# Optimization experiments

Hardware: AMD Instinct MI355X
Metric: run time of the kernel (lower is better)

Reference implementation:

```python
import jax, jax.numpy as jnp
import numpy as np

B, T, V, D = 4, 2048, 2048, 512

def setup_inputs() -> dict:
    key = jax.random.key(0)
    ks = jax.random.split(key, 8)
    x = jax.random.normal(ks[0], (B, T, V), dtype=jnp.float32)
    Wq = 0.02 * jax.random.normal(ks[1], (V, D), dtype=jnp.float32)
    Wk = 0.02 * jax.random.normal(ks[2], (3, V, D), dtype=jnp.float32)
    Wv = 0.02 * jax.random.normal(ks[3], (3, V, D), dtype=jnp.float32)
    Wo = 0.02 * jax.random.normal(ks[4], (D, V), dtype=jnp.float32)
    Wg = 0.02 * jax.random.normal(ks[5], (V, 3), dtype=jnp.float32)
    decay_logits = jnp.array([0.0, 3.0, 5.0], dtype=jnp.float32)
    out_scale = jnp.float32(0.1)
    return {"x": x, "Wq": Wq, "Wk": Wk, "Wv": Wv, "Wo": Wo, "Wg": Wg,
            "decay_logits": decay_logits, "out_scale": out_scale}

def reference(x, Wq, Wk, Wv, Wo, Wg, decay_logits, out_scale):
    # x: [B, T, V]
    Tn = x.shape[1]
    q = x @ Wq                                   # [B, T, D]
    gate = jax.nn.softmax(x @ Wg, axis=-1)       # [B, T, 3]
    pos = jnp.arange(Tn)
    diff = pos[None, :] - pos[:, None]           # diff[i, j] = j - i (as in torch code)
    causal = (diff > 0).astype(x.dtype)          # nonzero when j > i (faithful to source)
    expn = jnp.maximum(diff - 1, 0).astype(x.dtype)  # [T, T]
    blended = jnp.zeros(q.shape, dtype=x.dtype)
    for i in range(3):  # small fixed loop over 3 scales
        k = x @ Wk[i]                            # [B, T, D]
        v = x @ Wv[i]                            # [B, T, D]
        decay = jax.nn.sigmoid(decay_logits[i])
        w = (decay ** expn) * causal             # [T, T] decay mask
        scores = jnp.einsum('btd,bsd->bts', q, k) * w[None]  # [B, T, T]
        retrieved = jnp.einsum('bts,bsd->btd', scores, v)     # [B, T, D]
        blended = blended + gate[..., i:i + 1] * retrieved
    return (blended @ Wo) * out_scale            # [B, T, V]
```

## Files before the change

### kernel.cpp

```cpp
#include <hip/hip_runtime.h>
#include <hip/hip_bf16.h>
#include <cstdint>

typedef __attribute__((ext_vector_type(8))) short short8;
typedef __attribute__((ext_vector_type(4))) float f32x4;

#define DEV static __device__ __forceinline__

DEV unsigned short f2bf(float f) {
  uint32_t u = __float_as_uint(f);
  uint32_t r = (u + 0x7FFFu + ((u >> 16) & 1u)) >> 16;
  return (unsigned short)r;
}
DEV float bf2f(unsigned short v) { return __uint_as_float((uint32_t)v << 16); }

DEV unsigned short to_bf(float v) { return f2bf(v); }
DEV unsigned short to_bf(unsigned short v) { return v; }

DEV void async_copy16(const unsigned short* g, unsigned short* l) {
  __builtin_amdgcn_global_load_lds(
      (const __attribute__((address_space(1))) void*)g,
      (__attribute__((address_space(3))) void*)l, 16, 0, 0);
}

DEV int xcd_swizzle(int orig, int nwg) {
  int q = nwg >> 3, r = nwg & 7;
  int xcd = orig & 7, idx = orig >> 3;
  return (xcd < r ? xcd * (q + 1) : r * (q + 1) + (xcd - r) * q) + idx;
}

DEV void band_info(const float* __restrict__ dl, int T, int scale_idx, int zb, int ZB,
                   long& off, int& W, float& l2d) {
  off = 0; W = 0; l2d = 0.f;
  #pragma unroll
  for (int i = 0; i < 3; ++i) {
    float dlv = dl[i];
    float dc = 1.f / (1.f + expf(-dlv));
    float l2 = log2f(dc);
    float bf_ = 16.f / fmaxf(-l2, 1e-9f) + 129.f;
    int bt = (bf_ >= (float)T) ? T : ((int)ceilf(bf_ / 128.f)) * 128;
    if (bt > T) bt = T;
    int Wi = min(bt + 128, T);
    if (i < scale_idx) off += (long)ZB * T * Wi;
    if (i == scale_idx) { W = Wi; l2d = l2; }
  }
  off += (long)zb * (long)T * W;
}

__global__ __launch_bounds__(256) void convert_gate(
    const float* __restrict__ x, const float* __restrict__ Wg,
    unsigned short* __restrict__ xb, float* __restrict__ gate) {
  const int row = blockIdx.x;
  const float* xr = x + (long)row * 2048;
  unsigned short* xo = xb + (long)row * 2048;
  const int tid = threadIdx.x;
  float a0 = 0.f, a1 = 0.f, a2 = 0.f;
  #pragma unroll
  for (int u = 0; u < 2; ++u) {
    int c = u * 1024 + tid * 4;
    float4 v = *(const float4*)&xr[c];
    ushort4 o;
    o.x = f2bf(v.x); o.y = f2bf(v.y); o.z = f2bf(v.z); o.w = f2bf(v.w);
    *(ushort4*)&xo[c] = o;
    float vv[4] = {v.x, v.y, v.z, v.w};
    #pragma unroll
    for (int e = 0; e < 4; ++e) {
      a0 += vv[e] * Wg[(c + e) * 3 + 0];
      a1 += vv[e] * Wg[(c + e) * 3 + 1];
      a2 += vv[e] * Wg[(c + e) * 3 + 2];
    }
  }
  #pragma unroll
  for (int off = 32; off; off >>= 1) {
    a0 += __shfl_xor(a0, off);
    a1 += __shfl_xor(a1, off);
    a2 += __shfl_xor(a2, off);
  }
  __shared__ float red[3][4];
  const int w = tid >> 6, lane = tid & 63;
  if (lane == 0) { red[0][w] = a0; red[1][w] = a1; red[2][w] = a2; }
  __syncthreads();
  if (tid == 0) {
    float s0 = red[0][0] + red[0][1] + red[0][2] + red[0][3];
    float s1 = red[1][0] + red[1][1] + red[1][2] + red[1][3];
    float s2 = red[2][0] + red[2][1] + red[2][2] + red[2][3];
    float m = fmaxf(s0, fmaxf(s1, s2));
    float e0 = expf(s0 - m), e1 = expf(s1 - m), e2 = expf(s2 - m);
    float s = 1.f / (e0 + e1 + e2);
    gate[row * 3 + 0] = e0 * s;
    gate[row * 3 + 1] = e1 * s;
    gate[row * 3 + 2] = e2 * s;
  }
}

__global__ __launch_bounds__(256) void transpose_qkv_weights(
    const float* __restrict__ Wq, const float* __restrict__ Wk,
    const float* __restrict__ Wv, unsigned short* __restrict__ wall,
    int V, int D) {
  __shared__ unsigned short tile[32][33];
  const int z = blockIdx.z;
  const float* src = (z == 0) ? Wq
                   : (z < 4) ? Wk + (long)(z - 1) * V * D
                             : Wv + (long)(z - 4) * V * D;
  unsigned short* dst = wall + (long)z * D * V;
  int c0 = blockIdx.x * 32, r0 = blockIdx.y * 32;
  int tx = threadIdx.x & 31, ty = threadIdx.x >> 5;
  #pragma unroll
  for (int k = 0; k < 4; k++) {
    int rr = ty + k * 8;
    tile[rr][tx] = f2bf(src[(long)(r0 + rr) * D + c0 + tx]);
  }
  __syncthreads();
  #pragma unroll
  for (int k = 0; k < 4; k++) {
    int cc = ty + k * 8;
    dst[(long)(c0 + cc) * V + r0 + tx] = tile[tx][cc];
  }
}

template<typename TIN>
__global__ __launch_bounds__(256) void transpose_to_bf16(const TIN* __restrict__ src,
                                                         unsigned short* __restrict__ dst,
                                                         int R, int C, int ldS,
                                                         long sS_lo, long sS_hi, int ZB,
                                                         long sD) {
  __shared__ unsigned short tile[32][33];
  int z = blockIdx.z;
  src += (long)(z % ZB) * sS_lo + (long)(z / ZB) * sS_hi;
  dst += (long)z * sD;
  int c0 = blockIdx.x * 32, r0 = blockIdx.y * 32;
  int tx = threadIdx.x & 31, ty = threadIdx.x >> 5;
  #pragma unroll
  for (int k = 0; k < 4; k++) {
    int rr = ty + k * 8;
    tile[rr][tx] = to_bf(src[(long)(r0 + rr) * ldS + c0 + tx]);
  }
  __syncthreads();
  #pragma unroll
  for (int k = 0; k < 4; k++) {
    int cc = ty + k * 8;
    dst[(long)(c0 + cc) * R + r0 + tx] = tile[tx][cc];
  }
}

__global__ __launch_bounds__(256) void sum3_bf16(const unsigned short* __restrict__ r,
                                                 long n, long stride,
                                                 unsigned short* __restrict__ out) {
  long i = ((long)blockIdx.x * 256 + threadIdx.x) * 8;
  if (i >= n) return;
  short8 v0 = *(const short8*)&r[i];
  short8 v1 = *(const short8*)&r[i + stride];
  short8 v2 = *(const short8*)&r[i + 2 * stride];
  short8 o;
  #pragma unroll
  for (int e = 0; e < 8; ++e) {
    float s = bf2f((unsigned short)v0[e]) + bf2f((unsigned short)v1[e]) +
              bf2f((unsigned short)v2[e]);
    o[e] = (short)f2bf(s);
  }
  *(short8*)&out[i] = o;
}

DEV void core128(const unsigned short* A, const unsigned short* Bt,
                 int lda, int ldb, int m0, int n0,
                 int kaoff, int kboff, int kstart, int kend,
                 unsigned short* ldsbuf, int w, int lane,
                 f32x4 (&acc)[4][4]) {
  const int rl = w * 8 + (lane >> 3);
  const int colel = ((lane & 7) ^ (lane >> 3)) << 3;
  const int lr = lane & 15, g = lane >> 4;
  const int wm = w >> 1, wn = w & 1;
  unsigned short* aBuf = ldsbuf;
  unsigned short* bBuf = ldsbuf + 8192;

  for (int k0 = kstart; k0 < kend; k0 += 64) {
    #pragma unroll
    for (int s = 0; s < 4; ++s)
      async_copy16(A + (long)(m0 + s * 32 + rl) * lda + kaoff + k0 + colel,
                   aBuf + ((s * 4096 + w * 1024) >> 1));
    #pragma unroll
    for (int s = 0; s < 4; ++s)
      async_copy16(Bt + (long)(n0 + s * 32 + rl) * ldb + kboff + k0 + colel,
                   bBuf + ((s * 4096 + w * 1024) >> 1));
    __syncthreads();
    #pragma unroll
    for (int ks = 0; ks < 2; ++ks) {
      const int cb = (ks * 64 + g * 16) ^ ((lr & 7) << 4);
      short8 af[4], bf[4];
      #pragma unroll
      for (int i = 0; i < 4; ++i)
        af[i] = *(const short8*)((const char*)aBuf + (wm * 64 + i * 16 + lr) * 128 + cb);
      #pragma unroll
      for (int j = 0; j < 4; ++j)
        bf[j] = *(const short8*)((const char*)bBuf + (wn * 64 + j * 16 + lr) * 128 + cb);
      #pragma unroll
      for (int i = 0; i < 4; ++i)
        #pragma unroll
        for (int j = 0; j < 4; ++j)
          acc[i][j] = __builtin_amdgcn_mfma_f32_16x16x32_bf16(af[i], bf[j], acc[i][j], 0, 0, 0);
    }
    __syncthreads();
  }
}

__global__ __launch_bounds__(256) void scores_kernel(
    const unsigned short* __restrict__ qkv, unsigned short* __restrict__ sbc,
    int T, int D, int NP, int B, const float* __restrict__ dl) {
  const int z = blockIdx.z;
  const int zb = z % B, scale = z / B;
  const int m0 = blockIdx.y * 128;
  long off; int W; float l2d;
  band_info(dl, T, scale, zb, B, off, W, l2d);
  const int n0_rel = blockIdx.x * 128;
  if (n0_rel >= W) return;
  const int n0 = m0 + n0_rel;
  if (n0 >= T) return;

  const unsigned short* A  = qkv + (long)zb * T * NP;
  const unsigned short* Bt = qkv + (long)zb * T * NP + (1 + scale) * 512;

  __shared__ __align__(16) unsigned short lds[16384];
  const int tid = threadIdx.x;
  const int w = tid >> 6, lane = tid & 63;
  const int lr = lane & 15, g = lane >> 4;
  const int wm = w >> 1, wn = w & 1;

  f32x4 acc[4][4];
  #pragma unroll
  for (int i = 0; i < 4; i++)
    #pragma unroll
    for (int j = 0; j < 4; j++) acc[i][j] = (f32x4){0.f, 0.f, 0.f, 0.f};

  core128(A, Bt, NP, NP, m0, n0, 0, 0, 0, D, lds, w, lane, acc);

  unsigned short* C = sbc + off;
  const int orow = m0 + wm * 64;
  const int ocol_rel = n0_rel + wn * 64;
  #pragma unroll
  for (int i = 0; i < 4; i++)
    #pragma unroll
    for (int j = 0; j < 4; j++)
      #pragma unroll
      for (int e = 0; e < 4; e++) {
        int t = orow + i * 16 + g * 4 + e;
        int s_rel = ocol_rel + j * 16 + lr;
        int s_abs = m0 + s_rel;
        float wgt = (s_abs > t) ? exp2f(l2d * (float)(s_abs - t - 1)) : 0.f;
        C[(long)t * W + s_rel] = f2bf(acc[i][j][e] * wgt);
      }
}

__global__ __launch_bounds__(256) void retr_kernel(
    const unsigned short* __restrict__ sbc, const unsigned short* __restrict__ vT3,
    unsigned short* __restrict__ ret3, const float* __restrict__ gate,
    int T, int D, int B, const float* __restrict__ dl) {
  const int z = blockIdx.z;
  const int zb = z % B, scale = z / B;
  const int m0 = blockIdx.y * 128;
  const int n0 = blockIdx.x * 128;
  long off; int W; float l2d;
  band_info(dl, T, scale, zb, B, off, W, l2d);
  const int kend = min(W, T - m0);

  const unsigned short* A  = sbc + off;
  const unsigned short* Bt = vT3 + (long)z * D * T;

  __shared__ __align__(16) unsigned short lds[16384];
  const int tid = threadIdx.x;
  const int w = tid >> 6, lane = tid & 63;
  const int lr = lane & 15, g = lane >> 4;
  const int wm = w >> 1, wn = w & 1;

  f32x4 acc[4][4];
  #pragma unroll
  for (int i = 0; i < 4; i++)
    #pragma unroll
    for (int j = 0; j < 4; j++) acc[i][j] = (f32x4){0.f, 0.f, 0.f, 0.f};

  core128(A, Bt, W, T, m0, n0, 0, m0, 0, kend, lds, w, lane, acc);

  unsigned short* C2 = ret3 + (long)z * T * D;
  const int orow = m0 + wm * 64;
  const int ocol = n0 + wn * 64;
  #pragma unroll
  for (int i = 0; i < 4; i++) {
    #pragma unroll
    for (int e = 0; e < 4; e++) {
      int t = orow + i * 16 + g * 4 + e;
      float gv = gate[((long)zb * T + t) * 3 + scale];
      #pragma unroll
      for (int j = 0; j < 4; j++) {
        int d = ocol + j * 16 + lr;
        C2[(long)t * D + d] = f2bf(gv * acc[i][j][e]);
      }
    }
  }
}

__global__ __launch_bounds__(256) void gemm128_scale(
    const unsigned short* __restrict__ A, const unsigned short* __restrict__ Bt,
    float* __restrict__ C, int M, int N, int K, int lda, int ldb, int ldc,
    const float* __restrict__ out_scale) {
  int nwg = gridDim.x * gridDim.y;
  int orig = blockIdx.y * gridDim.x + blockIdx.x;
  int wg = xcd_swizzle(orig, nwg);
  const int m0 = (wg / gridDim.x) * 128;
  const int n0 = (wg % gridDim.x) * 128;

  __shared__ __align__(16) unsigned short lds[16384];
  const int tid = threadIdx.x;
  const int w = tid >> 6, lane = tid & 63;
  const int lr = lane & 15, g = lane >> 4;
  const int wm = w >> 1, wn = w & 1;

  f32x4 acc[4][4];
  #pragma unroll
  for (int i = 0; i < 4; i++)
    #pragma unroll
    for (int j = 0; j < 4; j++) acc[i][j] = (f32x4){0.f, 0.f, 0.f, 0.f};

  core128(A, Bt, lda, ldb, m0, n0, 0, 0, 0, K, lds, w, lane, acc);

  const float sc = *out_scale;
  const int orow = m0 + wm * 64;
  const int ocol = n0 + wn * 64;
  #pragma unroll
  for (int i = 0; i < 4; i++)
    #pragma unroll
    for (int j = 0; j < 4; j++)
      #pragma unroll
      for (int e = 0; e < 4; e++) {
        int r = orow + i * 16 + g * 4 + e;
        int c = ocol + j * 16 + lr;
        C[(long)r * ldc + c] = acc[i][j][e] * sc;
      }
}

enum { EPI_BF16 = 0, EPI_SCALE_F32 = 3 };

DEV void stage_pair(const unsigned short* P, int ldp, int base, int k0,
                    int w, int rl, int colel, unsigned short* dst, int s0) {
  async_copy16(P + (long)(base + s0 * 64 + rl) * ldp + k0 + colel,
               dst + ((s0 * 8192 + w * 1024) >> 1));
  async_copy16(P + (long)(base + (s0 + 1) * 64 + rl) * ldp + k0 + colel,
               dst + (((s0 + 1) * 8192 + w * 1024) >> 1));
}

DEV void ds_read_A4(const unsigned short* As, int wm, int lr, int cb, int h,
                    short8 (&af)[4]) {
  #pragma unroll
  for (int ii = 0; ii < 4; ++ii)
    af[ii] = *(const short8*)((const char*)As + (wm * 128 + (h * 4 + ii) * 16 + lr) * 128 + cb);
}

DEV void ds_read_B4(const unsigned short* Bs, int wn, int lr, int cb, short8 (&bf)[4]) {
  #pragma unroll
  for (int jj = 0; jj < 4; ++jj)
    bf[jj] = *(const short8*)((const char*)Bs + (wn * 64 + jj * 16 + lr) * 128 + cb);
}

DEV void mfma16(const short8 (&af)[4], const short8 (&bf)[4], int h, f32x4 (&acc)[8][4]) {
  __builtin_amdgcn_s_setprio(1);
  #pragma unroll
  for (int ii = 0; ii < 4; ++ii)
    #pragma unroll
    for (int jj = 0; jj < 4; ++jj)
      acc[h * 4 + ii][jj] =
          __builtin_amdgcn_mfma_f32_16x16x32_bf16(af[ii], bf[jj], acc[h * 4 + ii][jj], 0, 0, 0);
  __builtin_amdgcn_s_setprio(0);
}

template<bool STAGE>
DEV void tile_phases(const unsigned short* As, const unsigned short* Bs,
                     const unsigned short* A, const unsigned short* Bt,
                     int lda, int ldb, int m0, int n0, int k1,
                     int w, int rl, int colel, unsigned short* bufn,
                     int wm, int wn, int lr, int g, f32x4 (&acc)[8][4]) {
  short8 afA[4], afB[4], bfA[4], bfB[4];
  const int cb0 = (g * 16) ^ ((lr & 7) << 4);
  const int cb1 = (64 + g * 16) ^ ((lr & 7) << 4);

  asm volatile("s_waitcnt vmcnt(0)" ::: "memory");
  __builtin_amdgcn_s_barrier();
  __builtin_amdgcn_sched_barrier(0);

  ds_read_A4(As, wm, lr, cb0, 0, afA);
  ds_read_B4(Bs, wn, lr, cb0, bfA);

  ds_read_A4(As, wm, lr, cb0, 1, afB);
  if (STAGE) {
    stage_pair(A, lda, m0, k1, w, rl, colel, bufn, 0);
    stage_pair(A, lda, m0, k1, w, rl, colel, bufn, 2);
  }
  asm volatile("s_waitcnt lgkmcnt(4)" ::: "memory");
  __builtin_amdgcn_sched_barrier(0);
  mfma16(afA, bfA, 0, acc);
  __builtin_amdgcn_s_barrier();

  ds_read_A4(As, wm, lr, cb1, 0, afA);
  ds_read_B4(Bs, wn, lr, cb1, bfB);
  if (STAGE) {
    stage_pair(Bt, ldb, n0, k1, w, rl, colel, bufn + 16384, 0);
    stage_pair(Bt, ldb, n0, k1, w, rl, colel, bufn + 16384, 2);
  }
  asm volatile("s_waitcnt lgkmcnt(8)" ::: "memory");
  __builtin_amdgcn_sched_barrier(0);
  mfma16(afB, bfA, 1, acc);
  __builtin_amdgcn_s_barrier();

  ds_read_A4(As, wm, lr, cb1, 1, afB);
  asm volatile("s_waitcnt lgkmcnt(4)" ::: "memory");
  __builtin_amdgcn_sched_barrier(0);
  mfma16(afA, bfB, 0, acc);
  __builtin_amdgcn_s_barrier();

  asm volatile("s_waitcnt lgkmcnt(0)" ::: "memory");
  __builtin_amdgcn_sched_barrier(0);
  mfma16(afB, bfB, 1, acc);
  __builtin_amdgcn_s_barrier();
}

DEV void stage_tile256(const unsigned short* A, const unsigned short* Bt,
                       int lda, int ldb, int m0, int n0, int k0,
                       int w, int rl, int colel, unsigned short* buf) {
  #pragma unroll
  for (int s = 0; s < 4; ++s)
    async_copy16(A + (long)(m0 + s * 64 + rl) * lda + k0 + colel,
                 buf + ((s * 8192 + w * 1024) >> 1));
  #pragma unroll
  for (int s = 0; s < 4; ++s)
    async_copy16(Bt + (long)(n0 + s * 64 + rl) * ldb + k0 + colel,
                 buf + 16384 + ((s * 8192 + w * 1024) >> 1));
}

template<int EPI, int SWZ>
__global__ __launch_bounds__(512) void gemm256(
    const unsigned short* __restrict__ A, const unsigned short* __restrict__ Bt,
    void* __restrict__ Cv, int M, int N, int K, int lda, int ldb, int ldc,
    const float* __restrict__ out_scale) {
  __shared__ __align__(16) unsigned short lds[65536];
  int m0, n0;
  {
    int gx = gridDim.x;
    int orig = blockIdx.y * gx + blockIdx.x;
    int wg = SWZ ? xcd_swizzle(orig, gx * gridDim.y) : orig;
    m0 = (wg / gx) * 256;
    n0 = (wg % gx) * 256;
  }
  const int tid = threadIdx.x;
  const int w = tid >> 6, lane = tid & 63;
  const int wm = w >> 2, wn = w & 3;
  const int lr = lane & 15, g = lane >> 4;
  const int rl = w * 8 + (lane >> 3);
  const int colel = ((lane & 7) ^ (lane >> 3)) << 3;

  f32x4 acc[8][4];
  #pragma unroll
  for (int i = 0; i < 8; ++i)
    #pragma unroll
    for (int j = 0; j < 4; ++j) acc[i][j] = (f32x4){0.f, 0.f, 0.f, 0.f};

  const int nkt = K >> 6;
  stage_tile256(A, Bt, lda, ldb, m0, n0, 0, w, rl, colel, lds);
  int cur = 0;
  for (int t = 0; t < nkt - 1; ++t) {
    const unsigned short* As = lds + (cur << 15);
    unsigned short* bufn = lds + ((cur ^ 1) << 15);
    tile_phases<true>(As, As + 16384, A, Bt, lda, ldb, m0, n0, (t + 1) << 6,
                      w, rl, colel, bufn, wm, wn, lr, g, acc);
    cur ^= 1;
  }
  {
    const unsigned short* As = lds + (cur << 15);
    tile_phases<false>(As, As + 16384, A, Bt, lda, ldb, m0, n0, 0,
                       w, rl, colel, nullptr, wm, wn, lr, g, acc);
  }

  const int orow = m0 + wm * 128;
  const int ocol = n0 + wn * 64;
  if (EPI == EPI_BF16) {
    unsigned short* C = (unsigned short*)Cv;
    #pragma unroll
    for (int i = 0; i < 8; ++i)
      #pragma unroll
      for (int j = 0; j < 4; ++j)
        #pragma unroll
        for (int e = 0; e < 4; ++e)
          C[(long)(orow + i * 16 + g * 4 + e) * ldc + ocol + j * 16 + lr] = f2bf(acc[i][j][e]);
  } else {
    float sc = *out_scale;
    float* C = (float*)Cv;
    #pragma unroll
    for (int i = 0; i < 8; ++i)
      #pragma unroll
      for (int j = 0; j < 4; ++j)
        #pragma unroll
        for (int e = 0; e < 4; ++e)
          C[(long)(orow + i * 16 + g * 4 + e) * ldc + ocol + j * 16 + lr] = acc[i][j][e] * sc;
  }
}

extern "C" void kernel_launch(void* const* d_in, const int* in_sizes, int n_in,
                              void* d_out, int out_size, void* d_ws, size_t ws_size,
                              hipStream_t stream) {
  const int B = 4, T = 2048, V = 2048, D = 512;
  const int M = B * T;
  const int NP = 7 * D;

  const float* x   = (const float*)d_in[0];
  const float* Wq  = (const float*)d_in[1];
  const float* Wk  = (const float*)d_in[2];
  const float* Wv  = (const float*)d_in[3];
  const float* Wo  = (const float*)d_in[4];
  const float* Wg  = (const float*)d_in[5];
  const float* dl  = (const float*)d_in[6];
  const float* osc = (const float*)d_in[7];

  char* p = (char*)d_ws;
  auto carve = [&](size_t bytes) -> void* {
    void* r = (void*)p;
    p += (bytes + 255) & ~(size_t)255;
    return r;
  };
  unsigned short* qkv = (unsigned short*)carve((size_t)M * NP * 2);
  unsigned short* woT = (unsigned short*)carve((size_t)V * D * 2);
  float*          gate = (float*)carve((size_t)M * 3 * 4);
  unsigned short* blb = (unsigned short*)carve((size_t)M * D * 2);
  char* S = (char*)carve((size_t)100663296);
  unsigned short* xb   = (unsigned short*)S;
  unsigned short* wall = (unsigned short*)(S + 33554432);
  unsigned short* vT3  = (unsigned short*)S;
  unsigned short* sbc  = (unsigned short*)(S + 25165824);
  unsigned short* ret3 = (unsigned short*)(S + 75497472);

  convert_gate<<<dim3(M), dim3(256), 0, stream>>>(x, Wg, xb, gate);
  transpose_qkv_weights<<<dim3(D / 32, V / 32, 7), dim3(256), 0, stream>>>(
      Wq, Wk, Wv, wall, V, D);
  transpose_to_bf16<float><<<dim3(V / 32, D / 32, 1), dim3(256), 0, stream>>>(
      Wo, woT, D, V, V, 0, 0, 1, 0);
  gemm256<EPI_BF16, 1><<<dim3(NP / 256, M / 256, 1), dim3(512), 0, stream>>>(
      xb, wall, qkv, M, NP, V, V, V, NP, nullptr);
  transpose_to_bf16<unsigned short><<<dim3(D / 32, T / 32, 3 * B), dim3(256), 0, stream>>>(
      qkv + 2048, vT3, T, D, NP, (long)T * NP, 512, B, (long)D * T);
  scores_kernel<<<dim3(16, T / 128, 3 * B), dim3(256), 0, stream>>>(
      qkv, sbc, T, D, NP, B, dl);
  retr_kernel<<<dim3(D / 128, T / 128, 3 * B), dim3(256), 0, stream>>>(
      sbc, vT3, ret3, gate, T, D, B, dl);
  sum3_bf16<<<dim3((unsigned)((long)M * D / 8 / 256)), dim3(256), 0, stream>>>(
      ret3, (long)M * D, (long)M * D, blb);
  gemm128_scale<<<dim3(V / 128, M / 128, 1), dim3(256), 0, stream>>>(
      blb, woT, (float*)d_out, M, V, D, D, D, V, osc);
}
```

Measured before the change: 330.1 us.

## Double-buffer LDS in core GEMM loop to overlap global loads with MFMA

Replaces the single-buffered 128x128 GEMM core with a double-buffered version that issues async global-to-LDS copies for the next K tile while MFMAs run on the current one. It also splits the work into two half-steps with manual waitcnt and barriers, and raises MFMA wave priority with s_setprio. LDS use per block doubles to 64KB, which may cut occupancy. Correctness now depends on the hand-written waitcnt and barrier ordering.

```diff
diff --git a/kernel.cpp b/kernel.cpp
--- a/kernel.cpp
+++ b/kernel.cpp
@@ -161,45 +161,84 @@
   *(short8*)&out[i] = o;
 }
 
-DEV void core128(const unsigned short* A, const unsigned short* Bt,
-                 int lda, int ldb, int m0, int n0,
-                 int kaoff, int kboff, int kstart, int kend,
-                 unsigned short* ldsbuf, int w, int lane,
-                 f32x4 (&acc)[4][4]) {
+DEV void rd4(const char* base, int rowbase, int lr, int cb, short8 (&f)[4]) {
+  #pragma unroll
+  for (int i = 0; i < 4; ++i)
+    f[i] = *(const short8*)(base + (rowbase + i * 16 + lr) * 128 + cb);
+}
+
+DEV void mm16(const short8 (&af)[4], const short8 (&bf)[4], f32x4 (&acc)[4][4]) {
+  __builtin_amdgcn_s_setprio(1);
+  #pragma unroll
+  for (int i = 0; i < 4; ++i)
+    #pragma unroll
+    for (int j = 0; j < 4; ++j)
+      acc[i][j] = __builtin_amdgcn_mfma_f32_16x16x32_bf16(af[i], bf[j], acc[i][j], 0, 0, 0);
+  __builtin_amdgcn_s_setprio(0);
+}
+
+DEV void core128db(const unsigned short* A, const unsigned short* Bt,
+                   int lda, int ldb, int m0, int n0,
+                   int kaoff, int kboff, int kstart, int kend,
+                   unsigned short* lds, int w, int lane,
+                   f32x4 (&acc)[4][4]) {
   const int rl = w * 8 + (lane >> 3);
   const int colel = ((lane & 7) ^ (lane >> 3)) << 3;
   const int lr = lane & 15, g = lane >> 4;
   const int wm = w >> 1, wn = w & 1;
-  unsigned short* aBuf = ldsbuf;
-  unsigned short* bBuf = ldsbuf + 8192;
-
-  for (int k0 = kstart; k0 < kend; k0 += 64) {
-    #pragma unroll
-    for (int s = 0; s < 4; ++s)
-      async_copy16(A + (long)(m0 + s * 32 + rl) * lda + kaoff + k0 + colel,
-                   aBuf + ((s * 4096 + w * 1024) >> 1));
-    #pragma unroll
-    for (int s = 0; s < 4; ++s)
-      async_copy16(Bt + (long)(n0 + s * 32 + rl) * ldb + kboff + k0 + colel,
-                   bBuf + ((s * 4096 + w * 1024) >> 1));
-    __syncthreads();
-    #pragma unroll
-    for (int ks = 0; ks < 2; ++ks) {
-      const int cb = (ks * 64 + g * 16) ^ ((lr & 7) << 4);
-      short8 af[4], bf[4];
-      #pragma unroll
-      for (int i = 0; i < 4; ++i)
-        af[i] = *(const short8*)((const char*)aBuf + (wm * 64 + i * 16 + lr) * 128 + cb);
-      #pragma unroll
-      for (int j = 0; j < 4; ++j)
-        bf[j] = *(const short8*)((const char*)bBuf + (wn * 64 + j * 16 + lr) * 128 + cb);
-      #pragma unroll
-      for (int i = 0; i < 4; ++i)
-        #pragma unroll
-        for (int j = 0; j < 4; ++j)
-          acc[i][j] = __builtin_amdgcn_mfma_f32_16x16x32_bf16(af[i], bf[j], acc[i][j], 0, 0, 0);
+  const int cb0 = (g * 16) ^ ((lr & 7) << 4);
+  const int cb1 = (64 + g * 16) ^ ((lr & 7) << 4);
+
+  const int nkt = (kend - kstart) >> 6;
+
+  #pragma unroll
+  for (int s = 0; s < 4; ++s)
+    async_copy16(A + (long)(m0 + s * 32 + rl) * lda + kaoff + kstart + colel,
+                 lds + ((s * 4096 + w * 1024) >> 1));
+  #pragma unroll
+  for (int s = 0; s < 4; ++s)
+    async_copy16(Bt + (long)(n0 + s * 32 + rl) * ldb + kboff + kstart + colel,
+                 lds + 8192 + ((s * 4096 + w * 1024) >> 1));
+
+  int cur = 0;
+  for (int t = 0; t < nkt; ++t) {
+    const char* aB = (const char*)(lds + cur * 16384);
+    const char* bB = aB + 16384;
+    unsigned short* bufn = lds + ((cur ^ 1) * 16384);
+    const bool more = (t + 1 < nkt);
+    const int k1 = kstart + ((t + 1) << 6);
+
+    asm volatile("s_waitcnt vmcnt(0)" ::: "memory");
+    __builtin_amdgcn_s_barrier();
+    __builtin_amdgcn_sched_barrier(0);
+
+    short8 af0[4], bf0[4], af1[4], bf1[4];
+    rd4(aB, wm * 64, lr, cb0, af0);
+    rd4(bB, wn * 64, lr, cb0, bf0);
+
+    rd4(aB, wm * 64, lr, cb1, af1);
+    rd4(bB, wn * 64, lr, cb1, bf1);
+    if (more) {
+      #pragma unroll
+      for (int s = 0; s < 4; ++s)
+        async_copy16(A + (long)(m0 + s * 32 + rl) * lda + kaoff + k1 + colel,
+                     bufn + ((s * 4096 + w * 1024) >> 1));
     }
-    __syncthreads();
+    asm volatile("s_waitcnt lgkmcnt(8)" ::: "memory");
+    __builtin_amdgcn_sched_barrier(0);
+    mm16(af0, bf0, acc);
+    __builtin_amdgcn_s_barrier();
+
+    if (more) {
+      #pragma unroll
+      for (int s = 0; s < 4; ++s)
+        async_copy16(Bt + (long)(n0 + s * 32 + rl) * ldb + kboff + k1 + colel,
+                     bufn + 8192 + ((s * 4096 + w * 1024) >> 1));
+    }
+    asm volatile("s_waitcnt lgkmcnt(0)" ::: "memory");
+    __builtin_amdgcn_sched_barrier(0);
+    mm16(af1, bf1, acc);
+    cur ^= 1;
   }
 }
 
@@ -219,7 +258,7 @@
   const unsigned short* A  = qkv + (long)zb * T * NP;
   const unsigned short* Bt = qkv + (long)zb * T * NP + (1 + scale) * 512;
 
-  __shared__ __align__(16) unsigned short lds[16384];
+  __shared__ __align__(16) unsigned short lds[32768];
   const int tid = threadIdx.x;
   const int w = tid >> 6, lane = tid & 63;
   const int lr = lane & 15, g = lane >> 4;
@@ -231,7 +270,7 @@
     #pragma unroll
     for (int j = 0; j < 4; j++) acc[i][j] = (f32x4){0.f, 0.f, 0.f, 0.f};
 
-  core128(A, Bt, NP, NP, m0, n0, 0, 0, 0, D, lds, w, lane, acc);
+  core128db(A, Bt, NP, NP, m0, n0, 0, 0, 0, D, lds, w, lane, acc);
 
   unsigned short* C = sbc + off;
   const int orow = m0 + wm * 64;
@@ -265,7 +304,7 @@
   const unsigned short* A  = sbc + off;
   const unsigned short* Bt = vT3 + (long)z * D * T;
 
-  __shared__ __align__(16) unsigned short lds[16384];
+  __shared__ __align__(16) unsigned short lds[32768];
   const int tid = threadIdx.x;
   const int w = tid >> 6, lane = tid & 63;
   const int lr = lane & 15, g = lane >> 4;
@@ -277,7 +316,7 @@
     #pragma unroll
     for (int j = 0; j < 4; j++) acc[i][j] = (f32x4){0.f, 0.f, 0.f, 0.f};
 
-  core128(A, Bt, W, T, m0, n0, 0, m0, 0, kend, lds, w, lane, acc);
+  core128db(A, Bt, W, T, m0, n0, 0, m0, 0, kend, lds, w, lane, acc);
 
   unsigned short* C2 = ret3 + (long)z * T * D;
   const int orow = m0 + wm * 64;
@@ -307,7 +346,7 @@
   const int m0 = (wg / gridDim.x) * 128;
   const int n0 = (wg % gridDim.x) * 128;
 
-  __shared__ __align__(16) unsigned short lds[16384];
+  __shared__ __align__(16) unsigned short lds[32768];
   const int tid = threadIdx.x;
   const int w = tid >> 6, lane = tid & 63;
   const int lr = lane & 15, g = lane >> 4;
@@ -319,7 +358,7 @@
     #pragma unroll
     for (int j = 0; j < 4; j++) acc[i][j] = (f32x4){0.f, 0.f, 0.f, 0.f};
 
-  core128(A, Bt, lda, ldb, m0, n0, 0, 0, 0, K, lds, w, lane, acc);
+  core128db(A, Bt, lda, ldb, m0, n0, 0, 0, 0, K, lds, w, lane, acc);
 
   const float sc = *out_scale;
   const int orow = m0 + wm * 64;
```

Result: no change. 324.1 us (-1.8%).
